# Optimization experiments

Hardware: AMD Instinct MI355X
Metric: run time of the kernel (lower is better)

The kernel has to match this reference:

```python
import jax, jax.numpy as jnp
import numpy as np

B, S, L = 8, 64, 6          # graphs, spatial side, orientation layers
K = 6                       # Chebyshev order
IN_D, HID, OUT_D = 3, 128, 10


def _grid_edges(num_graphs, s, l):
    b, o, y, x = np.meshgrid(np.arange(num_graphs), np.arange(l), np.arange(s), np.arange(s), indexing='ij')
    nid = ((b * l + o) * s + y) * s + x  # linear node id, [B,L,s,s]
    srcs, dsts = [], []
    def add(a, c):
        srcs.append(a.ravel()); dsts.append(c.ravel())
    add(nid[..., :-1], nid[..., 1:]); add(nid[..., 1:], nid[..., :-1])                 # x-neighbors
    add(nid[:, :, :-1, :], nid[:, :, 1:, :]); add(nid[:, :, 1:, :], nid[:, :, :-1, :])  # y-neighbors
    nxt = np.roll(nid, -1, axis=1)                                                     # orientation ring
    add(nid, nxt); add(nxt, nid)
    return np.stack([np.concatenate(srcs), np.concatenate(dsts)]).astype(np.int32)


def _cluster_spatial(num_graphs, s, l):
    b, o, y, x = np.meshgrid(np.arange(num_graphs), np.arange(l), np.arange(s), np.arange(s), indexing='ij')
    h = s // 2
    return (((b * l + o) * h + y // 2) * h + x // 2).ravel().astype(np.int32)


def setup_inputs() -> dict:
    key = jax.random.key(0)
    ks = jax.random.split(key, 20)
    inp = {}
    N1 = B * L * S * S
    inp['x'] = jax.random.normal(ks[0], (N1, IN_D), jnp.float32)
    for i, s in enumerate([S, S // 2, S // 4]):
        ei = _grid_edges(B, s, L)
        inp[f'edge_index{i+1}'] = jnp.asarray(ei)
        inp[f'edge_attr{i+1}'] = jax.random.uniform(ks[1 + i], (ei.shape[1],), jnp.float32, 0.1, 1.0)
    inp['cluster1'] = jnp.asarray(_cluster_spatial(B, S, L))
    inp['cluster2'] = jnp.asarray(_cluster_spatial(B, S // 2, L))
    inp['cluster3'] = jnp.asarray(_cluster_spatial(B, S // 4, L))
    s4 = S // 8
    b, o, y, x = np.meshgrid(np.arange(B), np.arange(L), np.arange(s4), np.arange(s4), indexing='ij')
    inp['cluster4'] = jnp.asarray(((b * s4 + y) * s4 + x).ravel().astype(np.int32))  # collapse orientation axis
    inp['batch_final'] = jnp.asarray(np.repeat(np.arange(B), s4 * s4).astype(np.int32))
    dims = [(IN_D, HID), (HID, HID), (HID, HID), (HID, HID), (HID, HID), (HID, OUT_D)]
    for i, (di, do) in enumerate(dims):
        inp[f'W{i+1}'] = jax.random.normal(ks[8 + i], (K, di, do), jnp.float32) / np.float32(np.sqrt(di * K))
        inp[f'b{i+1}'] = jnp.zeros((do,), jnp.float32)
    for i in range(5):
        inp[f'gamma{i+1}'] = jnp.ones((HID,), jnp.float32)
        inp[f'beta{i+1}'] = jnp.zeros((HID,), jnp.float32)
    return inp


def _cheb_conv(x, ei, ea, W, b):
    # Chebyshev polynomial graph conv: out = sum_k T_k(L) x @ W_k + b,
    # with T0=x, T1=Lx, Tk = 2 L T_{k-1} - T_{k-2}; L applied via edge gather/scatter.
    src, dst = ei[0], ei[1]
    n = x.shape[0]
    def lap(v):
        return jax.ops.segment_sum(ea[:, None] * v[src], dst, num_segments=n)
    Tx0 = x
    out = Tx0 @ W[0]
    Tx1 = lap(x)
    out = out + Tx1 @ W[1]
    for k in range(2, W.shape[0]):
        Tx2 = 2.0 * lap(Tx1) - Tx0
        out = out + Tx2 @ W[k]
        Tx0, Tx1 = Tx1, Tx2
    return out + b


def _bn(x, g, bt):
    # BatchNorm1d in training mode (batch statistics, biased variance, eps=1e-5)
    mu = x.mean(0)
    var = x.var(0)
    return g * (x - mu) * jax.lax.rsqrt(var + 1e-5) + bt


def reference(x, edge_index1, edge_attr1, edge_index2, edge_attr2, edge_index3, edge_attr3, cluster1, cluster2, cluster3, cluster4, batch_final, W1, b1, W2, b2, W3, b3, W4, b4, W5, b5, W6, b6, gamma1, beta1, gamma2, beta2, gamma3, beta3, gamma4, beta4, gamma5, beta5):
    h = jax.nn.relu(_bn(_cheb_conv(x, edge_index1, edge_attr1, W1, b1), gamma1, beta1))
    h = jax.nn.relu(_bn(_cheb_conv(h, edge_index1, edge_attr1, W2, b2), gamma2, beta2))
    h = jax.ops.segment_max(h, cluster1, num_segments=B * L * (S // 2) ** 2)
    h = jax.nn.relu(_bn(_cheb_conv(h, edge_index2, edge_attr2, W3, b3), gamma3, beta3))
    h = jax.nn.relu(_bn(_cheb_conv(h, edge_index2, edge_attr2, W4, b4), gamma4, beta4))
    h = jax.ops.segment_max(h, cluster2, num_segments=B * L * (S // 4) ** 2)
    h = jax.nn.relu(_bn(_cheb_conv(h, edge_index3, edge_attr3, W5, b5), gamma5, beta5))
    h = jax.nn.relu(_cheb_conv(h, edge_index3, edge_attr3, W6, b6))
    h = jax.ops.segment_max(h, cluster3, num_segments=B * L * (S // 8) ** 2)   # spatial pool 3
    h = jax.ops.segment_max(h, cluster4, num_segments=B * (S // 8) ** 2)        # orientation pool
    g = jax.ops.segment_max(h, batch_final, num_segments=B)                     # global max pool
    return jax.nn.log_softmax(g, axis=1)
```

## Files before the change

### kernel.cpp

```cpp
#include <hip/hip_runtime.h>
#include <math.h>

#define L_OR 6
#define N_BL 48

typedef unsigned short u16;
typedef __attribute__((ext_vector_type(8))) short s8v;
typedef __attribute__((ext_vector_type(4))) float f4v;

#define N1 196608
#define N2 49152
#define N3 12288

__device__ u16   g_cat[(size_t)N1 * 768 + 1024];
__device__ u16   g_O[(size_t)N1 * 128];
__device__ float g_Tt[5 * (size_t)N1 * 3];
__device__ u16   g_Bt[128 * 768 + 8192];
__device__ u16   g_W6t[16 * 768];
__device__ float g_wt1[(size_t)N1 * 8];
__device__ float g_wt2[(size_t)N2 * 8];
__device__ float g_wt3[(size_t)N3 * 8];
__device__ float g_O10[(size_t)N3 * 10];
__device__ float g_p3[3072 * 10];
__device__ float g_p4[512 * 10];
__device__ float g_part[1536 * 256];
__device__ float g_part2[64 * 256];
__device__ float g_mean[128];
__device__ float g_inv[128];

__device__ __forceinline__ float b2f(u16 v) {
    return __uint_as_float(((unsigned)v) << 16);
}
__device__ __forceinline__ u16 f2b(float f) {
    unsigned u = __float_as_uint(f);
    return (u16)((u + 0x7FFFu + ((u >> 16) & 1u)) >> 16);
}

template<int S>
__global__ __launch_bounds__(256)
void eaprep(float* __restrict__ wtab, const float* __restrict__ ea)
{
    const int NN = N_BL * S * S;
    int n = blockIdx.x * 256 + threadIdx.x;
    if (n >= NN) return;
    int x = n % S, y = (n / S) % S, g = n / (S * S);
    int o = g % L_OR, b = g / L_OR;
    const int szx = N_BL * S * (S - 1);
    const int basex = (g * S + y) * (S - 1);
    float wxm = (x > 0)     ? ea[basex + x - 1] : 0.f;
    float wxp = (x < S - 1) ? ea[szx + basex + x] : 0.f;
    float wym = (y > 0)     ? ea[2 * szx + (g * (S - 1) + y - 1) * S + x] : 0.f;
    float wyp = (y < S - 1) ? ea[3 * szx + (g * (S - 1) + y) * S + x] : 0.f;
    int op_ = (o == 0) ? L_OR - 1 : o - 1;
    int on_ = (o == L_OR - 1) ? 0 : o + 1;
    int sp = ((b * L_OR + op_) * S + y) * S + x;
    int sn = ((b * L_OR + on_) * S + y) * S + x;
    float wom = ea[4 * szx + sp];
    float wop = ea[4 * szx + N_BL * S * S + n];
    float* w = wtab + (size_t)n * 8;
    w[0] = wxm; w[1] = wxp; w[2] = wym; w[3] = wyp; w[4] = wom; w[5] = wop;
    ((int*)w)[6] = sp - n;
    ((int*)w)[7] = sn - n;
}

template<int S>
__global__ __launch_bounds__(256)
void lap128b(u16* __restrict__ cat, int outSlot, int inSlot, int tppSlot,
             const float* __restrict__ wtab, float alpha)
{
    const int NN = N_BL * S * S;
    int node = blockIdx.x * 16 + (threadIdx.x >> 4);
    int c8   = threadIdx.x & 15;

    float4 wa = *(const float4*)(wtab + (size_t)node * 8);
    float4 wb = *(const float4*)(wtab + (size_t)node * 8 + 4);
    int dsp = __float_as_int(wb.z);
    int dsn = __float_as_int(wb.w);

    int sxm = (node > 0)      ? node - 1 : 0;
    int sxp = (node < NN - 1) ? node + 1 : node;
    int sym = (node >= S)     ? node - S : node;
    int syp = (node < NN - S) ? node + S : node;

    const int chOff = inSlot * 128 + c8 * 8;
    float a[8] = {0.f, 0.f, 0.f, 0.f, 0.f, 0.f, 0.f, 0.f};
    auto gather = [&](int src, float w) {
        s8v v = *(const s8v*)(cat + (size_t)src * 768 + chOff);
#pragma unroll
        for (int j = 0; j < 8; ++j) a[j] += w * b2f((u16)v[j]);
    };
    gather(sxm, wa.x);
    gather(sxp, wa.y);
    gather(sym, wa.z);
    gather(syp, wa.w);
    gather(node + dsp, wb.x);
    gather(node + dsn, wb.y);

    float r[8];
#pragma unroll
    for (int j = 0; j < 8; ++j) r[j] = alpha * a[j];
    if (tppSlot >= 0) {
        s8v t = *(const s8v*)(cat + (size_t)node * 768 + tppSlot * 128 + c8 * 8);
#pragma unroll
        for (int j = 0; j < 8; ++j) r[j] -= b2f((u16)t[j]);
    }
    uint4 ov;
    asm("v_cvt_pk_bf16_f32 %0, %1, %2" : "=v"(ov.x) : "v"(r[0]), "v"(r[1]));
    asm("v_cvt_pk_bf16_f32 %0, %1, %2" : "=v"(ov.y) : "v"(r[2]), "v"(r[3]));
    asm("v_cvt_pk_bf16_f32 %0, %1, %2" : "=v"(ov.z) : "v"(r[4]), "v"(r[5]));
    asm("v_cvt_pk_bf16_f32 %0, %1, %2" : "=v"(ov.w) : "v"(r[6]), "v"(r[7]));
    *(uint4*)(cat + (size_t)node * 768 + outSlot * 128 + c8 * 8) = ov;
}

template<int S>
__global__ __launch_bounds__(256)
void lap3_kernel(float* __restrict__ out, const float* __restrict__ in,
                 const float* __restrict__ tpp, const float* __restrict__ wtab,
                 float alpha)
{
    const int NN = N_BL * S * S;
    int n = blockIdx.x * 256 + threadIdx.x;
    if (n >= NN) return;
    float4 wa = *(const float4*)(wtab + (size_t)n * 8);
    float4 wb = *(const float4*)(wtab + (size_t)n * 8 + 4);
    int dsp = __float_as_int(wb.z);
    int dsn = __float_as_int(wb.w);
    int sxm = (n > 0)      ? n - 1 : 0;
    int sxp = (n < NN - 1) ? n + 1 : n;
    int sym = (n >= S)     ? n - S : n;
    int syp = (n < NN - S) ? n + S : n;

    float a0 = 0.f, a1 = 0.f, a2 = 0.f;
    auto gather = [&](int src, float w) {
        a0 += w * in[src * 3 + 0];
        a1 += w * in[src * 3 + 1];
        a2 += w * in[src * 3 + 2];
    };
    gather(sxm, wa.x); gather(sxp, wa.y); gather(sym, wa.z); gather(syp, wa.w);
    gather(n + dsp, wb.x); gather(n + dsn, wb.y);

    float r0 = alpha * a0, r1 = alpha * a1, r2 = alpha * a2;
    if (tpp) { r0 -= tpp[n * 3 + 0]; r1 -= tpp[n * 3 + 1]; r2 -= tpp[n * 3 + 2]; }
    out[n * 3 + 0] = r0; out[n * 3 + 1] = r1; out[n * 3 + 2] = r2;
}

__global__ __launch_bounds__(256)
void gemm_mfma_cat(u16* __restrict__ O, const u16* __restrict__ A,
                   const u16* __restrict__ Bf, const float* __restrict__ bias,
                   float* __restrict__ partials)
{
    __shared__ u16 Bs[2][8192];
    const int tid  = threadIdx.x;
    const int wave = tid >> 6;
    const int lane = tid & 63;
    const int lrow = lane & 15;
    const int kg   = lane >> 4;
    const int r0   = blockIdx.x * 128 + wave * 32;

    const u16* A0 = A + (size_t)(r0 + lrow) * 768 + kg * 8;
    const u16* A1 = A0 + (size_t)16 * 768;

    f4v acc[2][8] = {};

#pragma unroll
    for (int i = 0; i < 4; ++i)
        *(s8v*)&Bs[0][i * 2048 + tid * 8] = *(const s8v*)(Bf + i * 2048 + tid * 8);
    s8v a00 = *(const s8v*)(A0);
    s8v a10 = *(const s8v*)(A1);
    s8v a01 = *(const s8v*)(A0 + 32);
    s8v a11 = *(const s8v*)(A1 + 32);
    __syncthreads();

#pragma unroll 1
    for (int p = 0; p < 12; ++p) {
        const int cur = p & 1, nxt = cur ^ 1;
        const u16* src = Bf + (p + 1) * 8192;
        s8v nb0 = *(const s8v*)(src + tid * 8);
        s8v nb1 = *(const s8v*)(src + 2048 + tid * 8);
        s8v nb2 = *(const s8v*)(src + 4096 + tid * 8);
        s8v nb3 = *(const s8v*)(src + 6144 + tid * 8);
        s8v na00 = *(const s8v*)(A0 + (p + 1) * 64);
        s8v na10 = *(const s8v*)(A1 + (p + 1) * 64);
        s8v na01 = *(const s8v*)(A0 + (p + 1) * 64 + 32);
        s8v na11 = *(const s8v*)(A1 + (p + 1) * 64 + 32);
#pragma unroll
        for (int ct = 0; ct < 8; ++ct) {
            s8v b = *(const s8v*)&Bs[cur][(ct * 64 + lane) * 8];
            acc[0][ct] = __builtin_amdgcn_mfma_f32_16x16x32_bf16(a00, b, acc[0][ct], 0, 0, 0);
            acc[1][ct] = __builtin_amdgcn_mfma_f32_16x16x32_bf16(a10, b, acc[1][ct], 0, 0, 0);
        }
#pragma unroll
        for (int ct = 0; ct < 8; ++ct) {
            s8v b = *(const s8v*)&Bs[cur][4096 + (ct * 64 + lane) * 8];
            acc[0][ct] = __builtin_amdgcn_mfma_f32_16x16x32_bf16(a01, b, acc[0][ct], 0, 0, 0);
            acc[1][ct] = __builtin_amdgcn_mfma_f32_16x16x32_bf16(a11, b, acc[1][ct], 0, 0, 0);
        }
        __syncthreads();
        *(s8v*)&Bs[nxt][tid * 8]        = nb0;
        *(s8v*)&Bs[nxt][2048 + tid * 8] = nb1;
        *(s8v*)&Bs[nxt][4096 + tid * 8] = nb2;
        *(s8v*)&Bs[nxt][6144 + tid * 8] = nb3;
        __syncthreads();
        a00 = na00; a10 = na10; a01 = na01; a11 = na11;
    }

    __shared__ float sred[4][2][8][16];
    float cs[8], cq[8];
#pragma unroll
    for (int ct = 0; ct < 8; ++ct) { cs[ct] = 0.f; cq[ct] = 0.f; }

#pragma unroll
    for (int s = 0; s < 2; ++s)
#pragma unroll
        for (int ct = 0; ct < 8; ++ct) {
            int col = ct * 16 + lrow;
            float bv = bias[col];
#pragma unroll
            for (int j = 0; j < 4; ++j) {
                int row = r0 + s * 16 + kg * 4 + j;
                float v = acc[s][ct][j] + bv;
                O[(size_t)row * 128 + col] = f2b(v);
                cs[ct] += v; cq[ct] += v * v;
            }
        }
#pragma unroll
    for (int ct = 0; ct < 8; ++ct) {
        cs[ct] += __shfl_xor(cs[ct], 16); cs[ct] += __shfl_xor(cs[ct], 32);
        cq[ct] += __shfl_xor(cq[ct], 16); cq[ct] += __shfl_xor(cq[ct], 32);
    }
    if (lane < 16) {
#pragma unroll
        for (int ct = 0; ct < 8; ++ct) {
            sred[wave][0][ct][lane] = cs[ct];
            sred[wave][1][ct][lane] = cq[ct];
        }
    }
    __syncthreads();
    if (threadIdx.x < 128) {
        int ct = threadIdx.x >> 4, lr = threadIdx.x & 15;
        float S = 0.f, Q = 0.f;
#pragma unroll
        for (int w = 0; w < 4; ++w) { S += sred[w][0][ct][lr]; Q += sred[w][1][ct][lr]; }
        partials[blockIdx.x * 256 + threadIdx.x]       = S;
        partials[blockIdx.x * 256 + 128 + threadIdx.x] = Q;
    }
}

__global__ __launch_bounds__(256)
void wprep(const float* __restrict__ W, u16* __restrict__ Bf, int base)
{
    int idx = blockIdx.x * 256 + threadIdx.x;
    int j    = idx & 7;
    int lane = (idx >> 3) & 63;
    int ct   = (idx >> 9) & 7;
    int k0s  = idx >> 12;
    int k    = k0s * 32 + (lane >> 4) * 8 + j;
    int col  = ct * 16 + (lane & 15);
    int slot = k >> 7, d = k & 127;
    int wk = slot - base; if (wk < 0) wk += 6;
    Bf[idx] = f2b(W[(size_t)wk * 16384 + d * 128 + col]);
}

__global__ __launch_bounds__(256)
void w6prep(const float* __restrict__ W, u16* __restrict__ W6t, int base)
{
    int idx = blockIdx.x * 256 + threadIdx.x;
    if (idx >= 16 * 768) return;
    int c = idx / 768, kk = idx % 768;
    int slot = kk >> 7, d = kk & 127;
    int wk = slot - base; if (wk < 0) wk += 6;
    W6t[idx] = (c < 10) ? f2b(W[(size_t)wk * 1280 + d * 10 + c]) : (u16)0;
}

__global__ __launch_bounds__(256)
void l1gemm(u16* __restrict__ O, const float* __restrict__ T0,
            const float* __restrict__ Tt, const float* __restrict__ W,
            const float* __restrict__ bias, float* __restrict__ partials)
{
    __shared__ float Ts[128][18];
    __shared__ float sh[2][128], sh2[2][128];
    int tid = threadIdx.x;
    int rbase = blockIdx.x * 128;
    for (int i = tid; i < 128 * 18; i += 256) {
        int r = i / 18, t = i % 18;
        int k = t / 3, j = t % 3;
        Ts[r][t] = (k == 0) ? T0[(size_t)(rbase + r) * 3 + j]
                            : Tt[(size_t)(k - 1) * N1 * 3 + (size_t)(rbase + r) * 3 + j];
    }
    __syncthreads();
    int c = tid & 127, h = tid >> 7;
    float w[18];
#pragma unroll
    for (int k = 0; k < 6; ++k)
#pragma unroll
        for (int j = 0; j < 3; ++j) w[k * 3 + j] = W[(size_t)k * 384 + j * 128 + c];
    float bv = bias[c];
    float S = 0.f, Q = 0.f;
    for (int i = 0; i < 64; ++i) {
        int r = h * 64 + i;
        float acc = bv;
#pragma unroll
        for (int t = 0; t < 18; ++t) acc += Ts[r][t] * w[t];
        O[(size_t)(rbase + r) * 128 + c] = f2b(acc);
        S += acc; Q += acc * acc;
    }
    sh[h][c] = S; sh2[h][c] = Q;
    __syncthreads();
    if (tid < 128) {
        partials[blockIdx.x * 256 + tid]       = sh[0][tid] + sh[1][tid];
        partials[blockIdx.x * 256 + 128 + tid] = sh2[0][tid] + sh2[1][tid];
    }
}

__global__ __launch_bounds__(256)
void out10_cat(float* __restrict__ O10, const u16* __restrict__ cat,
               const u16* __restrict__ W6t, const float* __restrict__ bias)
{
    int col = threadIdx.x & 15;
    int row = blockIdx.x * 16 + (threadIdx.x >> 4);
    const u16* a = cat + (size_t)row * 768;
    const u16* w = W6t + (size_t)col * 768;
    float acc = 0.f;
#pragma unroll 4
    for (int k0 = 0; k0 < 768; k0 += 8) {
        s8v av = *(const s8v*)(a + k0);
        s8v wv = *(const s8v*)(w + k0);
#pragma unroll
        for (int j = 0; j < 8; ++j)
            acc += b2f((u16)av[j]) * b2f((u16)wv[j]);
    }
    if (col < 10)
        O10[(size_t)row * 10 + col] = fmaxf(acc + bias[col], 0.f);
}

__global__ __launch_bounds__(256)
void bn_reduce1(const float* __restrict__ partials, int nblk,
                float* __restrict__ part2)
{
    int tid = threadIdx.x;
    float S = 0.f;
#pragma unroll 4
    for (int b = blockIdx.x; b < nblk; b += 64)
        S += partials[(size_t)b * 256 + tid];
    part2[blockIdx.x * 256 + tid] = S;
}

__global__ __launch_bounds__(256)
void bn_finalize2(const float* __restrict__ part2, int N,
                  float* __restrict__ meanb, float* __restrict__ invstd)
{
    int tid = threadIdx.x;
    int c = tid & 127, h = tid >> 7;
    float S = 0.f, Q = 0.f;
#pragma unroll 8
    for (int b = h; b < 64; b += 2) {
        S += part2[b * 256 + c];
        Q += part2[b * 256 + 128 + c];
    }
    __shared__ float shS[2][128], shQ[2][128];
    shS[h][c] = S; shQ[h][c] = Q;
    __syncthreads();
    if (tid < 128) {
        float Sa = shS[0][tid] + shS[1][tid];
        float Qa = shQ[0][tid] + shQ[1][tid];
        float inv_n = 1.f / (float)N;
        float mu = Sa * inv_n;
        float var = Qa * inv_n - mu * mu;
        meanb[tid] = mu;
        invstd[tid] = rsqrtf(var + 1e-5f);
    }
}

__global__ __launch_bounds__(256)
void bn_apply_cat8(const u16* __restrict__ O, u16* __restrict__ cat, int slot,
                   const float* __restrict__ meanb, const float* __restrict__ invstd,
                   const float* __restrict__ g, const float* __restrict__ bt)
{
    int idx = blockIdx.x * 256 + threadIdx.x;
    int c8 = idx & 15;
    size_t row = idx >> 4;
    s8v v = *(const s8v*)(O + row * 128 + c8 * 8);
    s8v ov;
#pragma unroll
    for (int j = 0; j < 8; ++j) {
        int c = c8 * 8 + j;
        float val = (b2f((u16)v[j]) - meanb[c]) * invstd[c] * g[c] + bt[c];
        ov[j] = (short)f2b(fmaxf(val, 0.f));
    }
    *(s8v*)(cat + row * 768 + slot * 128 + c8 * 8) = ov;
}

__global__ __launch_bounds__(256)
void bn_apply_pool8(const u16* __restrict__ O, u16* __restrict__ cat, int outSlot,
                    int s, int Nout,
                    const float* __restrict__ meanb, const float* __restrict__ invstd,
                    const float* __restrict__ g, const float* __restrict__ bt)
{
    int idx = blockIdx.x * 256 + threadIdx.x;
    if (idx >= Nout * 16) return;
    int c8 = idx & 15;
    int n2 = idx >> 4;
    int h  = s >> 1;
    int x2 = n2 % h;
    int y2 = (n2 / h) % h;
    int gg = n2 / (h * h);
    int base = (gg * s + 2 * y2) * s + 2 * x2;
    s8v v0 = *(const s8v*)(O + (size_t)base * 128 + c8 * 8);
    s8v v1 = *(const s8v*)(O + (size_t)(base + 1) * 128 + c8 * 8);
    s8v v2 = *(const s8v*)(O + (size_t)(base + s) * 128 + c8 * 8);
    s8v v3 = *(const s8v*)(O + (size_t)(base + s + 1) * 128 + c8 * 8);
    s8v ov;
#pragma unroll
    for (int j = 0; j < 8; ++j) {
        int c = c8 * 8 + j;
        float sc = invstd[c] * g[c];
        float so = bt[c] - meanb[c] * sc;
        float m =          b2f((u16)v0[j]) * sc + so;
        m = fmaxf(m, b2f((u16)v1[j]) * sc + so);
        m = fmaxf(m, b2f((u16)v2[j]) * sc + so);
        m = fmaxf(m, b2f((u16)v3[j]) * sc + so);
        ov[j] = (short)f2b(fmaxf(m, 0.f));
    }
    *(s8v*)(cat + (size_t)n2 * 768 + outSlot * 128 + c8 * 8) = ov;
}

__global__ __launch_bounds__(256)
void pool_spatial(float* __restrict__ out, const float* __restrict__ in,
                  int s, int D, int Nout)
{
    int idx = blockIdx.x * 256 + threadIdx.x;
    if (idx >= Nout * D) return;
    int c  = idx % D;
    int n2 = idx / D;
    int h  = s >> 1;
    int x2 = n2 % h;
    int y2 = (n2 / h) % h;
    int g  = n2 / (h * h);
    int base = (g * s + 2 * y2) * s + 2 * x2;
    float m = in[(size_t)base * D + c];
    m = fmaxf(m, in[(size_t)(base + 1) * D + c]);
    m = fmaxf(m, in[(size_t)(base + s) * D + c]);
    m = fmaxf(m, in[(size_t)(base + s + 1) * D + c]);
    out[(size_t)n2 * D + c] = m;
}

__global__ __launch_bounds__(256)
void pool_orient(float* __restrict__ out, const float* __restrict__ in)
{
    int idx = blockIdx.x * 256 + threadIdx.x;
    if (idx >= 512 * 10) return;
    int c = idx % 10;
    int n = idx / 10;
    int x = n % 8, y = (n / 8) % 8, b = n / 64;
    float m = -INFINITY;
    for (int o = 0; o < L_OR; ++o)
        m = fmaxf(m, in[(size_t)((((b * L_OR + o) * 8 + y) * 8 + x)) * 10 + c]);
    out[idx] = m;
}

__global__ __launch_bounds__(128)
void global_pool_logsoftmax(const float* __restrict__ in, float* __restrict__ out)
{
    __shared__ float G[8][10];
    __shared__ float rowm[8], rowl[8];
    int t = threadIdx.x;
    if (t < 80) {
        int b = t / 10, c = t % 10;
        float m = -INFINITY;
        for (int p = 0; p < 64; ++p)
            m = fmaxf(m, in[(size_t)(b * 64 + p) * 10 + c]);
        G[b][c] = m;
    }
    __syncthreads();
    if (t < 8) {
        float m = -INFINITY;
        for (int c = 0; c < 10; ++c) m = fmaxf(m, G[t][c]);
        float s = 0.f;
        for (int c = 0; c < 10; ++c) s += expf(G[t][c] - m);
        rowm[t] = m; rowl[t] = logf(s);
    }
    __syncthreads();
    if (t < 80) {
        int b = t / 10, c = t % 10;
        out[t] = G[b][c] - rowm[b] - rowl[b];
    }
}

static void launch_lapb(u16* cat, int os, int is, int ts, const float* wtab,
                        int S, int N, float alpha, hipStream_t st)
{
    dim3 grid(N / 16), block(256);
    if (S == 64)      hipLaunchKernelGGL(lap128b<64>, grid, block, 0, st, cat, os, is, ts, wtab, alpha);
    else if (S == 32) hipLaunchKernelGGL(lap128b<32>, grid, block, 0, st, cat, os, is, ts, wtab, alpha);
    else              hipLaunchKernelGGL(lap128b<16>, grid, block, 0, st, cat, os, is, ts, wtab, alpha);
}

static void cheb_laps(u16* cat, int base, const float* wtab, int S, int N, hipStream_t st)
{
    for (int k = 1; k < 6; ++k) {
        int os = (k + base) % 6;
        int is = (k - 1 + base) % 6;
        int ts = (k >= 2) ? (k - 2 + base) % 6 : -1;
        launch_lapb(cat, os, is, ts, wtab, S, N, (k == 1) ? 1.f : 2.f, st);
    }
}

static void bn_reduce(float* part, float* part2, int nblk, int N,
                      float* meanb, float* invstd, hipStream_t st)
{
    hipLaunchKernelGGL(bn_reduce1, dim3(64), dim3(256), 0, st, part, nblk, part2);
    hipLaunchKernelGGL(bn_finalize2, dim3(1), dim3(256), 0, st, part2, N, meanb, invstd);
}

extern "C" void kernel_launch(void* const* d_in, const int* in_sizes, int n_in,
                              void* d_out, int out_size, void* d_ws, size_t ws_size,
                              hipStream_t stream)
{
    const float* x   = (const float*)d_in[0];
    const float* ea1 = (const float*)d_in[2];
    const float* ea2 = (const float*)d_in[4];
    const float* ea3 = (const float*)d_in[6];
    const float* W1  = (const float*)d_in[12];
    const float* b1  = (const float*)d_in[13];
    const float* W2  = (const float*)d_in[14];
    const float* b2  = (const float*)d_in[15];
    const float* W3  = (const float*)d_in[16];
    const float* b3  = (const float*)d_in[17];
    const float* W4  = (const float*)d_in[18];
    const float* b4  = (const float*)d_in[19];
    const float* W5  = (const float*)d_in[20];
    const float* b5  = (const float*)d_in[21];
    const float* W6  = (const float*)d_in[22];
    const float* b6  = (const float*)d_in[23];
    const float* g1  = (const float*)d_in[24];
    const float* be1 = (const float*)d_in[25];
    const float* g2  = (const float*)d_in[26];
    const float* be2 = (const float*)d_in[27];
    const float* g3  = (const float*)d_in[28];
    const float* be3 = (const float*)d_in[29];
    const float* g4  = (const float*)d_in[30];
    const float* be4 = (const float*)d_in[31];
    const float* g5  = (const float*)d_in[32];
    const float* be5 = (const float*)d_in[33];

    u16 *cat, *O, *Bt, *W6t;
    float *Tt, *O10, *p3, *p4, *part, *part2, *meanb, *invstd, *wt1, *wt2, *wt3;
    if (hipGetSymbolAddress((void**)&cat, HIP_SYMBOL(g_cat)) != hipSuccess) return;
    if (hipGetSymbolAddress((void**)&O,   HIP_SYMBOL(g_O))   != hipSuccess) return;
    if (hipGetSymbolAddress((void**)&Tt,  HIP_SYMBOL(g_Tt))  != hipSuccess) return;
    if (hipGetSymbolAddress((void**)&Bt,  HIP_SYMBOL(g_Bt))  != hipSuccess) return;
    if (hipGetSymbolAddress((void**)&W6t, HIP_SYMBOL(g_W6t)) != hipSuccess) return;
    if (hipGetSymbolAddress((void**)&O10, HIP_SYMBOL(g_O10)) != hipSuccess) return;
    if (hipGetSymbolAddress((void**)&p3,  HIP_SYMBOL(g_p3))  != hipSuccess) return;
    if (hipGetSymbolAddress((void**)&p4,  HIP_SYMBOL(g_p4))  != hipSuccess) return;
    if (hipGetSymbolAddress((void**)&part,   HIP_SYMBOL(g_part))  != hipSuccess) return;
    if (hipGetSymbolAddress((void**)&part2,  HIP_SYMBOL(g_part2)) != hipSuccess) return;
    if (hipGetSymbolAddress((void**)&meanb,  HIP_SYMBOL(g_mean))  != hipSuccess) return;
    if (hipGetSymbolAddress((void**)&invstd, HIP_SYMBOL(g_inv))   != hipSuccess) return;
    if (hipGetSymbolAddress((void**)&wt1, HIP_SYMBOL(g_wt1)) != hipSuccess) return;
    if (hipGetSymbolAddress((void**)&wt2, HIP_SYMBOL(g_wt2)) != hipSuccess) return;
    if (hipGetSymbolAddress((void**)&wt3, HIP_SYMBOL(g_wt3)) != hipSuccess) return;

    dim3 blk(256);

    hipLaunchKernelGGL(eaprep<64>, dim3(N1 / 256), blk, 0, stream, wt1, ea1);
    hipLaunchKernelGGL(eaprep<32>, dim3(N2 / 256), blk, 0, stream, wt2, ea2);
    hipLaunchKernelGGL(eaprep<16>, dim3(N3 / 256), blk, 0, stream, wt3, ea3);

    {
        float* t1 = Tt;
        float* t2 = Tt + (size_t)N1 * 3;
        float* t3 = Tt + (size_t)2 * N1 * 3;
        float* t4 = Tt + (size_t)3 * N1 * 3;
        float* t5 = Tt + (size_t)4 * N1 * 3;
        dim3 gl((N1 + 255) / 256);
        hipLaunchKernelGGL(lap3_kernel<64>, gl, blk, 0, stream, t1, x,  (const float*)nullptr, wt1, 1.f);
        hipLaunchKernelGGL(lap3_kernel<64>, gl, blk, 0, stream, t2, t1, x,  wt1, 2.f);
        hipLaunchKernelGGL(lap3_kernel<64>, gl, blk, 0, stream, t3, t2, t1, wt1, 2.f);
        hipLaunchKernelGGL(lap3_kernel<64>, gl, blk, 0, stream, t4, t3, t2, wt1, 2.f);
        hipLaunchKernelGGL(lap3_kernel<64>, gl, blk, 0, stream, t5, t4, t3, wt1, 2.f);
        hipLaunchKernelGGL(l1gemm, dim3(N1 / 128), blk, 0, stream, O, x, Tt, W1, b1, part);
    }
    bn_reduce(part, part2, N1 / 128, N1, meanb, invstd, stream);
    hipLaunchKernelGGL(bn_apply_cat8, dim3(N1 / 16), blk, 0, stream,
                       O, cat, 0, meanb, invstd, g1, be1);

    hipLaunchKernelGGL(wprep, dim3(384), blk, 0, stream, W2, Bt, 0);
    cheb_laps(cat, 0, wt1, 64, N1, stream);
    hipLaunchKernelGGL(gemm_mfma_cat, dim3(N1 / 128), blk, 0, stream, O, cat, Bt, b2, part);
    bn_reduce(part, part2, N1 / 128, N1, meanb, invstd, stream);
    hipLaunchKernelGGL(bn_apply_pool8, dim3(N2 / 16), blk, 0, stream,
                       O, cat, 5, 64, N2, meanb, invstd, g2, be2);

    hipLaunchKernelGGL(wprep, dim3(384), blk, 0, stream, W3, Bt, 5);
    cheb_laps(cat, 5, wt2, 32, N2, stream);
    hipLaunchKernelGGL(gemm_mfma_cat, dim3(N2 / 128), blk, 0, stream, O, cat, Bt, b3, part);
    bn_reduce(part, part2, N2 / 128, N2, meanb, invstd, stream);
    hipLaunchKernelGGL(bn_apply_cat8, dim3(N2 / 16), blk, 0, stream,
                       O, cat, 0, meanb, invstd, g3, be3);

    hipLaunchKernelGGL(wprep, dim3(384), blk, 0, stream, W4, Bt, 0);
    cheb_laps(cat, 0, wt2, 32, N2, stream);
    hipLaunchKernelGGL(gemm_mfma_cat, dim3(N2 / 128), blk, 0, stream, O, cat, Bt, b4, part);
    bn_reduce(part, part2, N2 / 128, N2, meanb, invstd, stream);
    hipLaunchKernelGGL(bn_apply_pool8, dim3(N3 / 16), blk, 0, stream,
                       O, cat, 5, 32, N3, meanb, invstd, g4, be4);

    hipLaunchKernelGGL(wprep, dim3(384), blk, 0, stream, W5, Bt, 5);
    cheb_laps(cat, 5, wt3, 16, N3, stream);
    hipLaunchKernelGGL(gemm_mfma_cat, dim3(N3 / 128), blk, 0, stream, O, cat, Bt, b5, part);
    bn_reduce(part, part2, N3 / 128, N3, meanb, invstd, stream);
    hipLaunchKernelGGL(bn_apply_cat8, dim3(N3 / 16), blk, 0, stream,
                       O, cat, 0, meanb, invstd, g5, be5);

    hipLaunchKernelGGL(w6prep, dim3(48), blk, 0, stream, W6, W6t, 0);
    cheb_laps(cat, 0, wt3, 16, N3, stream);
    hipLaunchKernelGGL(out10_cat, dim3(N3 / 16), blk, 0, stream, O10, cat, W6t, b6);

    hipLaunchKernelGGL(pool_spatial, dim3((3072 * 10 + 255) / 256), blk, 0, stream,
                       p3, O10, 16, 10, 3072);
    hipLaunchKernelGGL(pool_orient, dim3((512 * 10 + 255) / 256), blk, 0, stream, p4, p3);
    hipLaunchKernelGGL(global_pool_logsoftmax, dim3(1), dim3(128), 0, stream,
                       p4, (float*)d_out);
}
```

Before: 795.1 us.

## Fuse BN-apply into first Laplacian, batch weight prep, and fuse pooling tail

Removes the separate bn_apply_cat8 pass by folding BN scale/offset and ReLU into a new lap1bn kernel, which writes both T0 and T1 straight from the GEMM output. Batches edge-attr and weight preparation into single launches done up front, with per-layer weight buffers. Fuses the three tail pooling kernels plus log-softmax into one block. Restructures the GEMM B-tile prefetch to hold two stages in registers. Fewer launches and one less full-feature read/write pass, at the cost of a tail kernel that runs on a single block and extra gather-side BN math repeated for each neighbor.

```diff
diff --git a/kernel.cpp b/kernel.cpp
--- a/kernel.cpp
+++ b/kernel.cpp
@@ -11,22 +11,21 @@
 #define N1 196608
 #define N2 49152
 #define N3 12288
+#define LSTRIDE 114688
 
 __device__ u16   g_cat[(size_t)N1 * 768 + 1024];
 __device__ u16   g_O[(size_t)N1 * 128];
 __device__ float g_Tt[5 * (size_t)N1 * 3];
-__device__ u16   g_Bt[128 * 768 + 8192];
+__device__ u16   g_Bt[4 * LSTRIDE];
 __device__ u16   g_W6t[16 * 768];
 __device__ float g_wt1[(size_t)N1 * 8];
 __device__ float g_wt2[(size_t)N2 * 8];
 __device__ float g_wt3[(size_t)N3 * 8];
 __device__ float g_O10[(size_t)N3 * 10];
-__device__ float g_p3[3072 * 10];
-__device__ float g_p4[512 * 10];
 __device__ float g_part[1536 * 256];
 __device__ float g_part2[64 * 256];
-__device__ float g_mean[128];
-__device__ float g_inv[128];
+__device__ float g_gsc[128];
+__device__ float g_gso[128];
 
 __device__ __forceinline__ float b2f(u16 v) {
     return __uint_as_float(((unsigned)v) << 16);
@@ -36,13 +35,17 @@
     return (u16)((u + 0x7FFFu + ((u >> 16) & 1u)) >> 16);
 }
 
-template<int S>
-__global__ __launch_bounds__(256)
-void eaprep(float* __restrict__ wtab, const float* __restrict__ ea)
-{
-    const int NN = N_BL * S * S;
-    int n = blockIdx.x * 256 + threadIdx.x;
-    if (n >= NN) return;
+__global__ __launch_bounds__(256)
+void eaprep_all(float* __restrict__ wt1, float* __restrict__ wt2,
+                float* __restrict__ wt3, const float* __restrict__ ea1,
+                const float* __restrict__ ea2, const float* __restrict__ ea3)
+{
+    int idx = blockIdx.x * 256 + threadIdx.x;
+    int S, n; float* wtab; const float* ea;
+    if (idx < N1)            { S = 64; wtab = wt1; ea = ea1; n = idx; }
+    else if (idx < N1 + N2)  { S = 32; wtab = wt2; ea = ea2; n = idx - N1; }
+    else if (idx < N1 + N2 + N3) { S = 16; wtab = wt3; ea = ea3; n = idx - N1 - N2; }
+    else return;
     int x = n % S, y = (n / S) % S, g = n / (S * S);
     int o = g % L_OR, b = g / L_OR;
     const int szx = N_BL * S * (S - 1);
@@ -76,7 +79,6 @@
     float4 wb = *(const float4*)(wtab + (size_t)node * 8 + 4);
     int dsp = __float_as_int(wb.z);
     int dsn = __float_as_int(wb.w);
-
     int sxm = (node > 0)      ? node - 1 : 0;
     int sxp = (node < NN - 1) ? node + 1 : node;
     int sym = (node >= S)     ? node - S : node;
@@ -89,12 +91,8 @@
 #pragma unroll
         for (int j = 0; j < 8; ++j) a[j] += w * b2f((u16)v[j]);
     };
-    gather(sxm, wa.x);
-    gather(sxp, wa.y);
-    gather(sym, wa.z);
-    gather(syp, wa.w);
-    gather(node + dsp, wb.x);
-    gather(node + dsn, wb.y);
+    gather(sxm, wa.x); gather(sxp, wa.y); gather(sym, wa.z); gather(syp, wa.w);
+    gather(node + dsp, wb.x); gather(node + dsn, wb.y);
 
     float r[8];
 #pragma unroll
@@ -110,6 +108,67 @@
     asm("v_cvt_pk_bf16_f32 %0, %1, %2" : "=v"(ov.z) : "v"(r[4]), "v"(r[5]));
     asm("v_cvt_pk_bf16_f32 %0, %1, %2" : "=v"(ov.w) : "v"(r[6]), "v"(r[7]));
     *(uint4*)(cat + (size_t)node * 768 + outSlot * 128 + c8 * 8) = ov;
+}
+
+template<int S>
+__global__ __launch_bounds__(256)
+void lap1bn(u16* __restrict__ cat, const u16* __restrict__ O,
+            int t0Slot, int t1Slot, const float* __restrict__ wtab,
+            const float* __restrict__ gsc, const float* __restrict__ gso)
+{
+    const int NN = N_BL * S * S;
+    int node = blockIdx.x * 16 + (threadIdx.x >> 4);
+    int c8   = threadIdx.x & 15;
+
+    float4 wa = *(const float4*)(wtab + (size_t)node * 8);
+    float4 wb = *(const float4*)(wtab + (size_t)node * 8 + 4);
+    int dsp = __float_as_int(wb.z);
+    int dsn = __float_as_int(wb.w);
+    int sxm = (node > 0)      ? node - 1 : 0;
+    int sxp = (node < NN - 1) ? node + 1 : node;
+    int sym = (node >= S)     ? node - S : node;
+    int syp = (node < NN - S) ? node + S : node;
+
+    float sc[8], so[8];
+    {
+        float4 s0 = *(const float4*)(gsc + c8 * 8);
+        float4 s1 = *(const float4*)(gsc + c8 * 8 + 4);
+        float4 o0 = *(const float4*)(gso + c8 * 8);
+        float4 o1 = *(const float4*)(gso + c8 * 8 + 4);
+        sc[0]=s0.x; sc[1]=s0.y; sc[2]=s0.z; sc[3]=s0.w;
+        sc[4]=s1.x; sc[5]=s1.y; sc[6]=s1.z; sc[7]=s1.w;
+        so[0]=o0.x; so[1]=o0.y; so[2]=o0.z; so[3]=o0.w;
+        so[4]=o1.x; so[5]=o1.y; so[6]=o1.z; so[7]=o1.w;
+    }
+
+    float a[8] = {0.f, 0.f, 0.f, 0.f, 0.f, 0.f, 0.f, 0.f};
+    auto gatherbn = [&](int src, float w) {
+        s8v v = *(const s8v*)(O + (size_t)src * 128 + c8 * 8);
+#pragma unroll
+        for (int j = 0; j < 8; ++j)
+            a[j] += w * fmaxf(b2f((u16)v[j]) * sc[j] + so[j], 0.f);
+    };
+    gatherbn(sxm, wa.x); gatherbn(sxp, wa.y); gatherbn(sym, wa.z); gatherbn(syp, wa.w);
+    gatherbn(node + dsp, wb.x); gatherbn(node + dsn, wb.y);
+
+    float t0[8];
+    {
+        s8v v = *(const s8v*)(O + (size_t)node * 128 + c8 * 8);
+#pragma unroll
+        for (int j = 0; j < 8; ++j)
+            t0[j] = fmaxf(b2f((u16)v[j]) * sc[j] + so[j], 0.f);
+    }
+    uint4 o0v, o1v;
+    asm("v_cvt_pk_bf16_f32 %0, %1, %2" : "=v"(o0v.x) : "v"(t0[0]), "v"(t0[1]));
+    asm("v_cvt_pk_bf16_f32 %0, %1, %2" : "=v"(o0v.y) : "v"(t0[2]), "v"(t0[3]));
+    asm("v_cvt_pk_bf16_f32 %0, %1, %2" : "=v"(o0v.z) : "v"(t0[4]), "v"(t0[5]));
+    asm("v_cvt_pk_bf16_f32 %0, %1, %2" : "=v"(o0v.w) : "v"(t0[6]), "v"(t0[7]));
+    asm("v_cvt_pk_bf16_f32 %0, %1, %2" : "=v"(o1v.x) : "v"(a[0]), "v"(a[1]));
+    asm("v_cvt_pk_bf16_f32 %0, %1, %2" : "=v"(o1v.y) : "v"(a[2]), "v"(a[3]));
+    asm("v_cvt_pk_bf16_f32 %0, %1, %2" : "=v"(o1v.z) : "v"(a[4]), "v"(a[5]));
+    asm("v_cvt_pk_bf16_f32 %0, %1, %2" : "=v"(o1v.w) : "v"(a[6]), "v"(a[7]));
+    *(uint4*)(cat + (size_t)node * 768 + t0Slot * 128 + c8 * 8) = o0v;
+    *(uint4*)(cat + (size_t)node * 768 + t1Slot * 128 + c8 * 8) = o1v;
 }
 
 template<int S>
@@ -162,47 +221,80 @@
 
     f4v acc[2][8] = {};
 
+#define COMPUTE(BUF, A00, A10, A01, A11)                                        \
+    {                                                                           \
+        _Pragma("unroll")                                                       \
+        for (int ct = 0; ct < 8; ++ct) {                                        \
+            s8v b = *(const s8v*)&Bs[BUF][(ct * 64 + lane) * 8];                \
+            acc[0][ct] = __builtin_amdgcn_mfma_f32_16x16x32_bf16(A00, b, acc[0][ct], 0, 0, 0); \
+            acc[1][ct] = __builtin_amdgcn_mfma_f32_16x16x32_bf16(A10, b, acc[1][ct], 0, 0, 0); \
+        }                                                                       \
+        _Pragma("unroll")                                                       \
+        for (int ct = 0; ct < 8; ++ct) {                                        \
+            s8v b = *(const s8v*)&Bs[BUF][4096 + (ct * 64 + lane) * 8];         \
+            acc[0][ct] = __builtin_amdgcn_mfma_f32_16x16x32_bf16(A01, b, acc[0][ct], 0, 0, 0); \
+            acc[1][ct] = __builtin_amdgcn_mfma_f32_16x16x32_bf16(A11, b, acc[1][ct], 0, 0, 0); \
+        }                                                                       \
+    }
+
 #pragma unroll
     for (int i = 0; i < 4; ++i)
         *(s8v*)&Bs[0][i * 2048 + tid * 8] = *(const s8v*)(Bf + i * 2048 + tid * 8);
+    s8v rX0 = *(const s8v*)(Bf + 8192 + tid * 8);
+    s8v rX1 = *(const s8v*)(Bf + 8192 + 2048 + tid * 8);
+    s8v rX2 = *(const s8v*)(Bf + 8192 + 4096 + tid * 8);
+    s8v rX3 = *(const s8v*)(Bf + 8192 + 6144 + tid * 8);
     s8v a00 = *(const s8v*)(A0);
     s8v a10 = *(const s8v*)(A1);
     s8v a01 = *(const s8v*)(A0 + 32);
     s8v a11 = *(const s8v*)(A1 + 32);
+    s8v rY0, rY1, rY2, rY3;
     __syncthreads();
 
 #pragma unroll 1
-    for (int p = 0; p < 12; ++p) {
-        const int cur = p & 1, nxt = cur ^ 1;
-        const u16* src = Bf + (p + 1) * 8192;
-        s8v nb0 = *(const s8v*)(src + tid * 8);
-        s8v nb1 = *(const s8v*)(src + 2048 + tid * 8);
-        s8v nb2 = *(const s8v*)(src + 4096 + tid * 8);
-        s8v nb3 = *(const s8v*)(src + 6144 + tid * 8);
-        s8v na00 = *(const s8v*)(A0 + (p + 1) * 64);
-        s8v na10 = *(const s8v*)(A1 + (p + 1) * 64);
-        s8v na01 = *(const s8v*)(A0 + (p + 1) * 64 + 32);
-        s8v na11 = *(const s8v*)(A1 + (p + 1) * 64 + 32);
-#pragma unroll
-        for (int ct = 0; ct < 8; ++ct) {
-            s8v b = *(const s8v*)&Bs[cur][(ct * 64 + lane) * 8];
-            acc[0][ct] = __builtin_amdgcn_mfma_f32_16x16x32_bf16(a00, b, acc[0][ct], 0, 0, 0);
-            acc[1][ct] = __builtin_amdgcn_mfma_f32_16x16x32_bf16(a10, b, acc[1][ct], 0, 0, 0);
+    for (int q = 0; q < 6; ++q) {
+        {
+            const int p = 2 * q;
+            const u16* src = Bf + (p + 2) * 8192;
+            rY0 = *(const s8v*)(src + tid * 8);
+            rY1 = *(const s8v*)(src + 2048 + tid * 8);
+            rY2 = *(const s8v*)(src + 4096 + tid * 8);
+            rY3 = *(const s8v*)(src + 6144 + tid * 8);
+            s8v na00 = *(const s8v*)(A0 + (p + 1) * 64);
+            s8v na10 = *(const s8v*)(A1 + (p + 1) * 64);
+            s8v na01 = *(const s8v*)(A0 + (p + 1) * 64 + 32);
+            s8v na11 = *(const s8v*)(A1 + (p + 1) * 64 + 32);
+            COMPUTE(0, a00, a10, a01, a11);
+            __syncthreads();
+            *(s8v*)&Bs[1][tid * 8]        = rX0;
+            *(s8v*)&Bs[1][2048 + tid * 8] = rX1;
+            *(s8v*)&Bs[1][4096 + tid * 8] = rX2;
+            *(s8v*)&Bs[1][6144 + tid * 8] = rX3;
+            __syncthreads();
+            a00 = na00; a10 = na10; a01 = na01; a11 = na11;
         }
-#pragma unroll
-        for (int ct = 0; ct < 8; ++ct) {
-            s8v b = *(const s8v*)&Bs[cur][4096 + (ct * 64 + lane) * 8];
-            acc[0][ct] = __builtin_amdgcn_mfma_f32_16x16x32_bf16(a01, b, acc[0][ct], 0, 0, 0);
-            acc[1][ct] = __builtin_amdgcn_mfma_f32_16x16x32_bf16(a11, b, acc[1][ct], 0, 0, 0);
+        {
+            const int p = 2 * q + 1;
+            const u16* src = Bf + (p + 2) * 8192;
+            rX0 = *(const s8v*)(src + tid * 8);
+            rX1 = *(const s8v*)(src + 2048 + tid * 8);
+            rX2 = *(const s8v*)(src + 4096 + tid * 8);
+            rX3 = *(const s8v*)(src + 6144 + tid * 8);
+            s8v na00 = *(const s8v*)(A0 + (p + 1) * 64);
+            s8v na10 = *(const s8v*)(A1 + (p + 1) * 64);
+            s8v na01 = *(const s8v*)(A0 + (p + 1) * 64 + 32);
+            s8v na11 = *(const s8v*)(A1 + (p + 1) * 64 + 32);
+            COMPUTE(1, a00, a10, a01, a11);
+            __syncthreads();
+            *(s8v*)&Bs[0][tid * 8]        = rY0;
+            *(s8v*)&Bs[0][2048 + tid * 8] = rY1;
+            *(s8v*)&Bs[0][4096 + tid * 8] = rY2;
+            *(s8v*)&Bs[0][6144 + tid * 8] = rY3;
+            __syncthreads();
+            a00 = na00; a10 = na10; a01 = na01; a11 = na11;
         }
-        __syncthreads();
-        *(s8v*)&Bs[nxt][tid * 8]        = nb0;
-        *(s8v*)&Bs[nxt][2048 + tid * 8] = nb1;
-        *(s8v*)&Bs[nxt][4096 + tid * 8] = nb2;
-        *(s8v*)&Bs[nxt][6144 + tid * 8] = nb3;
-        __syncthreads();
-        a00 = na00; a10 = na10; a01 = na01; a11 = na11;
-    }
+    }
+#undef COMPUTE
 
     __shared__ float sred[4][2][8][16];
     float cs[8], cq[8];
@@ -247,8 +339,13 @@
 }
 
 __global__ __launch_bounds__(256)
-void wprep(const float* __restrict__ W, u16* __restrict__ Bf, int base)
-{
+void wprep_all(const float* __restrict__ W2, const float* __restrict__ W3,
+               const float* __restrict__ W4, const float* __restrict__ W5,
+               u16* __restrict__ Bf)
+{
+    int l = blockIdx.y;
+    const float* W = (l == 0) ? W2 : (l == 1) ? W3 : (l == 2) ? W4 : W5;
+    int base = (l & 1) ? 5 : 0;
     int idx = blockIdx.x * 256 + threadIdx.x;
     int j    = idx & 7;
     int lane = (idx >> 3) & 63;
@@ -258,7 +355,7 @@
     int col  = ct * 16 + (lane & 15);
     int slot = k >> 7, d = k & 127;
     int wk = slot - base; if (wk < 0) wk += 6;
-    Bf[idx] = f2b(W[(size_t)wk * 16384 + d * 128 + col]);
+    Bf[(size_t)l * LSTRIDE + idx] = f2b(W[(size_t)wk * 16384 + d * 128 + col]);
 }
 
 __global__ __launch_bounds__(256)
@@ -347,7 +444,8 @@
 
 __global__ __launch_bounds__(256)
 void bn_finalize2(const float* __restrict__ part2, int N,
-                  float* __restrict__ meanb, float* __restrict__ invstd)
+                  const float* __restrict__ g, const float* __restrict__ bt,
+                  float* __restrict__ gsc, float* __restrict__ gso)
 {
     int tid = threadIdx.x;
     int c = tid & 127, h = tid >> 7;
@@ -366,35 +464,17 @@
         float inv_n = 1.f / (float)N;
         float mu = Sa * inv_n;
         float var = Qa * inv_n - mu * mu;
-        meanb[tid] = mu;
-        invstd[tid] = rsqrtf(var + 1e-5f);
-    }
-}
-
-__global__ __launch_bounds__(256)
-void bn_apply_cat8(const u16* __restrict__ O, u16* __restrict__ cat, int slot,
-                   const float* __restrict__ meanb, const float* __restrict__ invstd,
-                   const float* __restrict__ g, const float* __restrict__ bt)
-{
-    int idx = blockIdx.x * 256 + threadIdx.x;
-    int c8 = idx & 15;
-    size_t row = idx >> 4;
-    s8v v = *(const s8v*)(O + row * 128 + c8 * 8);
-    s8v ov;
-#pragma unroll
-    for (int j = 0; j < 8; ++j) {
-        int c = c8 * 8 + j;
-        float val = (b2f((u16)v[j]) - meanb[c]) * invstd[c] * g[c] + bt[c];
-        ov[j] = (short)f2b(fmaxf(val, 0.f));
-    }
-    *(s8v*)(cat + row * 768 + slot * 128 + c8 * 8) = ov;
+        float is = rsqrtf(var + 1e-5f);
+        float sc = is * g[tid];
+        gsc[tid] = sc;
+        gso[tid] = bt[tid] - mu * sc;
+    }
 }
 
 __global__ __launch_bounds__(256)
 void bn_apply_pool8(const u16* __restrict__ O, u16* __restrict__ cat, int outSlot,
                     int s, int Nout,
-                    const float* __restrict__ meanb, const float* __restrict__ invstd,
-                    const float* __restrict__ g, const float* __restrict__ bt)
+                    const float* __restrict__ gsc, const float* __restrict__ gso)
 {
     int idx = blockIdx.x * 256 + threadIdx.x;
     if (idx >= Nout * 16) return;
@@ -413,8 +493,7 @@
 #pragma unroll
     for (int j = 0; j < 8; ++j) {
         int c = c8 * 8 + j;
-        float sc = invstd[c] * g[c];
-        float so = bt[c] - meanb[c] * sc;
+        float sc = gsc[c], so = gso[c];
         float m =          b2f((u16)v0[j]) * sc + so;
         m = fmaxf(m, b2f((u16)v1[j]) * sc + so);
         m = fmaxf(m, b2f((u16)v2[j]) * sc + so);
@@ -424,51 +503,31 @@
     *(s8v*)(cat + (size_t)n2 * 768 + outSlot * 128 + c8 * 8) = ov;
 }
 
-__global__ __launch_bounds__(256)
-void pool_spatial(float* __restrict__ out, const float* __restrict__ in,
-                  int s, int D, int Nout)
-{
-    int idx = blockIdx.x * 256 + threadIdx.x;
-    if (idx >= Nout * D) return;
-    int c  = idx % D;
-    int n2 = idx / D;
-    int h  = s >> 1;
-    int x2 = n2 % h;
-    int y2 = (n2 / h) % h;
-    int g  = n2 / (h * h);
-    int base = (g * s + 2 * y2) * s + 2 * x2;
-    float m = in[(size_t)base * D + c];
-    m = fmaxf(m, in[(size_t)(base + 1) * D + c]);
-    m = fmaxf(m, in[(size_t)(base + s) * D + c]);
-    m = fmaxf(m, in[(size_t)(base + s + 1) * D + c]);
-    out[(size_t)n2 * D + c] = m;
-}
-
-__global__ __launch_bounds__(256)
-void pool_orient(float* __restrict__ out, const float* __restrict__ in)
-{
-    int idx = blockIdx.x * 256 + threadIdx.x;
-    if (idx >= 512 * 10) return;
-    int c = idx % 10;
-    int n = idx / 10;
-    int x = n % 8, y = (n / 8) % 8, b = n / 64;
-    float m = -INFINITY;
-    for (int o = 0; o < L_OR; ++o)
-        m = fmaxf(m, in[(size_t)((((b * L_OR + o) * 8 + y) * 8 + x)) * 10 + c]);
-    out[idx] = m;
-}
-
-__global__ __launch_bounds__(128)
-void global_pool_logsoftmax(const float* __restrict__ in, float* __restrict__ out)
-{
+__global__ __launch_bounds__(512)
+void tail_fused(const float* __restrict__ O10, float* __restrict__ out)
+{
+    __shared__ float p4[512][10];
     __shared__ float G[8][10];
     __shared__ float rowm[8], rowl[8];
     int t = threadIdx.x;
+    for (int i = t; i < 5120; i += 512) {
+        int c = i % 10, n = i / 10;
+        int x = n & 7, y = (n >> 3) & 7, b = n >> 6;
+        float m = -INFINITY;
+        for (int o = 0; o < L_OR; ++o) {
+            int base = ((b * L_OR + o) * 16 + 2 * y) * 16 + 2 * x;
+            m = fmaxf(m, O10[(size_t)base * 10 + c]);
+            m = fmaxf(m, O10[(size_t)(base + 1) * 10 + c]);
+            m = fmaxf(m, O10[(size_t)(base + 16) * 10 + c]);
+            m = fmaxf(m, O10[(size_t)(base + 17) * 10 + c]);
+        }
+        p4[n][c] = m;
+    }
+    __syncthreads();
     if (t < 80) {
         int b = t / 10, c = t % 10;
         float m = -INFINITY;
-        for (int p = 0; p < 64; ++p)
-            m = fmaxf(m, in[(size_t)(b * 64 + p) * 10 + c]);
+        for (int p = 0; p < 64; ++p) m = fmaxf(m, p4[b * 64 + p][c]);
         G[b][c] = m;
     }
     __syncthreads();
@@ -495,21 +554,38 @@
     else              hipLaunchKernelGGL(lap128b<16>, grid, block, 0, st, cat, os, is, ts, wtab, alpha);
 }
 
-static void cheb_laps(u16* cat, int base, const float* wtab, int S, int N, hipStream_t st)
+static void cheb_laps_b5(u16* cat, const float* wtab, int S, int N, hipStream_t st)
 {
     for (int k = 1; k < 6; ++k) {
-        int os = (k + base) % 6;
-        int is = (k - 1 + base) % 6;
-        int ts = (k >= 2) ? (k - 2 + base) % 6 : -1;
+        int os = (k + 5) % 6;
+        int is = (k - 1 + 5) % 6;
+        int ts = (k >= 2) ? (k - 2 + 5) % 6 : -1;
         launch_lapb(cat, os, is, ts, wtab, S, N, (k == 1) ? 1.f : 2.f, st);
     }
 }
 
+static void cheb_laps_2to5(u16* cat, const float* wtab, int S, int N, hipStream_t st)
+{
+    for (int k = 2; k < 6; ++k)
+        launch_lapb(cat, k, k - 1, k - 2, wtab, S, N, 2.f, st);
+}
+
+static void launch_lap1bn(u16* cat, const u16* O, const float* wtab,
+                          const float* gsc, const float* gso,
+                          int S, int N, hipStream_t st)
+{
+    dim3 grid(N / 16), block(256);
+    if (S == 64)      hipLaunchKernelGGL(lap1bn<64>, grid, block, 0, st, cat, O, 0, 1, wtab, gsc, gso);
+    else if (S == 32) hipLaunchKernelGGL(lap1bn<32>, grid, block, 0, st, cat, O, 0, 1, wtab, gsc, gso);
+    else              hipLaunchKernelGGL(lap1bn<16>, grid, block, 0, st, cat, O, 0, 1, wtab, gsc, gso);
+}
+
 static void bn_reduce(float* part, float* part2, int nblk, int N,
-                      float* meanb, float* invstd, hipStream_t st)
+                      const float* g, const float* bt,
+                      float* gsc, float* gso, hipStream_t st)
 {
     hipLaunchKernelGGL(bn_reduce1, dim3(64), dim3(256), 0, st, part, nblk, part2);
-    hipLaunchKernelGGL(bn_finalize2, dim3(1), dim3(256), 0, st, part2, N, meanb, invstd);
+    hipLaunchKernelGGL(bn_finalize2, dim3(1), dim3(256), 0, st, part2, N, g, bt, gsc, gso);
 }
 
 extern "C" void kernel_launch(void* const* d_in, const int* in_sizes, int n_in,
@@ -544,28 +620,27 @@
     const float* be5 = (const float*)d_in[33];
 
     u16 *cat, *O, *Bt, *W6t;
-    float *Tt, *O10, *p3, *p4, *part, *part2, *meanb, *invstd, *wt1, *wt2, *wt3;
+    float *Tt, *O10, *part, *part2, *gsc, *gso, *wt1, *wt2, *wt3;
     if (hipGetSymbolAddress((void**)&cat, HIP_SYMBOL(g_cat)) != hipSuccess) return;
     if (hipGetSymbolAddress((void**)&O,   HIP_SYMBOL(g_O))   != hipSuccess) return;
     if (hipGetSymbolAddress((void**)&Tt,  HIP_SYMBOL(g_Tt))  != hipSuccess) return;
     if (hipGetSymbolAddress((void**)&Bt,  HIP_SYMBOL(g_Bt))  != hipSuccess) return;
     if (hipGetSymbolAddress((void**)&W6t, HIP_SYMBOL(g_W6t)) != hipSuccess) return;
     if (hipGetSymbolAddress((void**)&O10, HIP_SYMBOL(g_O10)) != hipSuccess) return;
-    if (hipGetSymbolAddress((void**)&p3,  HIP_SYMBOL(g_p3))  != hipSuccess) return;
-    if (hipGetSymbolAddress((void**)&p4,  HIP_SYMBOL(g_p4))  != hipSuccess) return;
-    if (hipGetSymbolAddress((void**)&part,   HIP_SYMBOL(g_part))  != hipSuccess) return;
-    if (hipGetSymbolAddress((void**)&part2,  HIP_SYMBOL(g_part2)) != hipSuccess) return;
-    if (hipGetSymbolAddress((void**)&meanb,  HIP_SYMBOL(g_mean))  != hipSuccess) return;
-    if (hipGetSymbolAddress((void**)&invstd, HIP_SYMBOL(g_inv))   != hipSuccess) return;
+    if (hipGetSymbolAddress((void**)&part,  HIP_SYMBOL(g_part))  != hipSuccess) return;
+    if (hipGetSymbolAddress((void**)&part2, HIP_SYMBOL(g_part2)) != hipSuccess) return;
+    if (hipGetSymbolAddress((void**)&gsc, HIP_SYMBOL(g_gsc)) != hipSuccess) return;
+    if (hipGetSymbolAddress((void**)&gso, HIP_SYMBOL(g_gso)) != hipSuccess) return;
     if (hipGetSymbolAddress((void**)&wt1, HIP_SYMBOL(g_wt1)) != hipSuccess) return;
     if (hipGetSymbolAddress((void**)&wt2, HIP_SYMBOL(g_wt2)) != hipSuccess) return;
     if (hipGetSymbolAddress((void**)&wt3, HIP_SYMBOL(g_wt3)) != hipSuccess) return;
 
     dim3 blk(256);
 
-    hipLaunchKernelGGL(eaprep<64>, dim3(N1 / 256), blk, 0, stream, wt1, ea1);
-    hipLaunchKernelGGL(eaprep<32>, dim3(N2 / 256), blk, 0, stream, wt2, ea2);
-    hipLaunchKernelGGL(eaprep<16>, dim3(N3 / 256), blk, 0, stream, wt3, ea3);
+    hipLaunchKernelGGL(eaprep_all, dim3((N1 + N2 + N3) / 256), blk, 0, stream,
+                       wt1, wt2, wt3, ea1, ea2, ea3);
+    hipLaunchKernelGGL(wprep_all, dim3(384, 4), blk, 0, stream, W2, W3, W4, W5, Bt);
+    hipLaunchKernelGGL(w6prep, dim3(48), blk, 0, stream, W6, W6t, 0);
 
     {
         float* t1 = Tt;
@@ -581,45 +656,33 @@
         hipLaunchKernelGGL(lap3_kernel<64>, gl, blk, 0, stream, t5, t4, t3, wt1, 2.f);
         hipLaunchKernelGGL(l1gemm, dim3(N1 / 128), blk, 0, stream, O, x, Tt, W1, b1, part);
     }
-    bn_reduce(part, part2, N1 / 128, N1, meanb, invstd, stream);
-    hipLaunchKernelGGL(bn_apply_cat8, dim3(N1 / 16), blk, 0, stream,
-                       O, cat, 0, meanb, invstd, g1, be1);
-
-    hipLaunchKernelGGL(wprep, dim3(384), blk, 0, stream, W2, Bt, 0);
-    cheb_laps(cat, 0, wt1, 64, N1, stream);
+    bn_reduce(part, part2, N1 / 128, N1, g1, be1, gsc, gso, stream);
+
+    launch_lap1bn(cat, O, wt1, gsc, gso, 64, N1, stream);
+    cheb_laps_2to5(cat, wt1, 64, N1, stream);
     hipLaunchKernelGGL(gemm_mfma_cat, dim3(N1 / 128), blk, 0, stream, O, cat, Bt, b2, part);
-    bn_reduce(part, part2, N1 / 128, N1, meanb, invstd, stream);
+    bn_reduce(part, part2, N1 / 128, N1, g2, be2, gsc, gso, stream);
     hipLaunchKernelGGL(bn_apply_pool8, dim3(N2 / 16), blk, 0, stream,
-                       O, cat, 5, 64, N2, meanb, invstd, g2, be2);
-
-    hipLaunchKernelGGL(wprep, dim3(384), blk, 0, stream, W3, Bt, 5);
-    cheb_laps(cat, 5, wt2, 32, N2, stream);
-    hipLaunchKernelGGL(gemm_mfma_cat, dim3(N2 / 128), blk, 0, stream, O, cat, Bt, b3, part);
-    bn_reduce(part, part2, N2 / 128, N2, meanb, invstd, stream);
-    hipLaunchKernelGGL(bn_apply_cat8, dim3(N2 / 16), blk, 0, stream,
-                       O, cat, 0, meanb, invstd, g3, be3);
-
-    hipLaunchKernelGGL(wprep, dim3(384), blk, 0, stream, W4, Bt, 0);
-    cheb_laps(cat, 0, wt2, 32, N2, stream);
-    hipLaunchKernelGGL(gemm_mfma_cat, dim3(N2 / 128), blk, 0, stream, O, cat, Bt, b4, part);
-    bn_reduce(part, part2, N2 / 128, N2, meanb, invstd, stream);
+                       O, cat, 5, 64, N2, gsc, gso);
+
+    cheb_laps_b5(cat, wt2, 32, N2, stream);
+    hipLaunchKernelGGL(gemm_mfma_cat, dim3(N2 / 128), blk, 0, stream, O, cat, Bt + 1 * LSTRIDE, b3, part);
+    bn_reduce(part, part2, N2 / 128, N2, g3, be3, gsc, gso, stream);
+
+    launch_lap1bn(cat, O, wt2, gsc, gso, 32, N2, stream);
+    cheb_laps_2to5(cat, wt2, 32, N2, stream);
+    hipLaunchKernelGGL(gemm_mfma_cat, dim3(N2 / 128), blk, 0, stream, O, cat, Bt + 2 * LSTRIDE, b4, part);
+    bn_reduce(part, part2, N2 / 128, N2, g4, be4, gsc, gso, stream);
     hipLaunchKernelGGL(bn_apply_pool8, dim3(N3 / 16), blk, 0, stream,
-                       O, cat, 5, 32, N3, meanb, invstd, g4, be4);
-
-    hipLaunchKernelGGL(wprep, dim3(384), blk, 0, stream, W5, Bt, 5);
-    cheb_laps(cat, 5, wt3, 16, N3, stream);
-    hipLaunchKernelGGL(gemm_mfma_cat, dim3(N3 / 128), blk, 0, stream, O, cat, Bt, b5, part);
-    bn_reduce(part, part2, N3 / 128, N3, meanb, invstd, stream);
-    hipLaunchKernelGGL(bn_apply_cat8, dim3(N3 / 16), blk, 0, stream,
-                       O, cat, 0, meanb, invstd, g5, be5);
-
-    hipLaunchKernelGGL(w6prep, dim3(48), blk, 0, stream, W6, W6t, 0);
-    cheb_laps(cat, 0, wt3, 16, N3, stream);
+                       O, cat, 5, 32, N3, gsc, gso);
+
+    cheb_laps_b5(cat, wt3, 16, N3, stream);
+    hipLaunchKernelGGL(gemm_mfma_cat, dim3(N3 / 128), blk, 0, stream, O, cat, Bt + 3 * LSTRIDE, b5, part);
+    bn_reduce(part, part2, N3 / 128, N3, g5, be5, gsc, gso, stream);
+
+    launch_lap1bn(cat, O, wt3, gsc, gso, 16, N3, stream);
+    cheb_laps_2to5(cat, wt3, 16, N3, stream);
     hipLaunchKernelGGL(out10_cat, dim3(N3 / 16), blk, 0, stream, O10, cat, W6t, b6);
 
-    hipLaunchKernelGGL(pool_spatial, dim3((3072 * 10 + 255) / 256), blk, 0, stream,
-                       p3, O10, 16, 10, 3072);
-    hipLaunchKernelGGL(pool_orient, dim3((512 * 10 + 255) / 256), blk, 0, stream, p4, p3);
-    hipLaunchKernelGGL(global_pool_logsoftmax, dim3(1), dim3(128), 0, stream,
-                       p4, (float*)d_out);
-}
+    hipLaunchKernelGGL(tail_fused, dim3(1), dim3(512), 0, stream, O10, (float*)d_out);
+}
```

Result: faster. 760.5 us (-4.4%).
